# Performance work log

Hardware: AMD Instinct MI355X
Metric: run time of the kernel (lower is better)

## Reference

```python
import jax, jax.numpy as jnp
import numpy as np

GRID_SIZE = 64
THRESHOLD = 1.0
SIGMA = 1.5
K_SHARP = 2.0


def _gaussian_kernel(sigma):
    ksize = max(int(4 * sigma) | 1, 3)
    x = jnp.arange(ksize, dtype=jnp.float32) - ksize // 2
    g1d = jnp.exp(-x ** 2 / (2.0 * sigma ** 2))
    g2d = g1d[None, :] * g1d[:, None]
    g2d = g2d / g2d.sum()
    return g2d[None, None]  # (1,1,k,k) OIHW


def setup_inputs() -> dict:
    key = jax.random.key(0)
    k1, k2, k3, k4 = jax.random.split(key, 4)
    B, V, P, N, MAXP = 4, 512, 8192, 2000, 8
    positions = jax.random.uniform(k1, (B, V, 2), dtype=jnp.float32) * 2.0 - 1.0
    pin_offsets = jax.random.normal(k2, (P, 2), dtype=jnp.float32) * 0.05
    net_to_pin = jax.random.randint(k3, (N, MAXP), 0, P, dtype=jnp.int32)
    pin_to_macro = jax.random.randint(k4, (P,), 0, V, dtype=jnp.int32)
    return {"positions": positions, "pin_offsets": pin_offsets,
            "net_to_pin": net_to_pin, "pin_to_macro": pin_to_macro}


def reference(positions, pin_offsets, net_to_pin, pin_to_macro):
    B = positions.shape[0]
    M = GRID_SIZE
    num_nets = net_to_pin.shape[0]

    # pin positions: (B, P, 2) -- no rotation (rotation_onehot=None branch)
    pin_pos = positions[:, pin_to_macro, :] + pin_offsets[None]

    # per-net bounding boxes over valid pins
    valid = net_to_pin >= 0                                  # (N, maxp)
    safe_idx = jnp.maximum(net_to_pin, 0)
    net_pin_pos = pin_pos[:, safe_idx, :]                    # (B, N, maxp, 2)
    mask = valid[None, :, :, None]
    bbox_max = jnp.max(jnp.where(mask, net_pin_pos, -1e9), axis=2)  # (B, N, 2)
    bbox_min = jnp.min(jnp.where(mask, net_pin_pos, 1e9), axis=2)

    # to grid coordinates
    bbox_max_g = (bbox_max + 1.0) * 0.5 * (M - 1)
    bbox_min_g = (bbox_min + 1.0) * 0.5 * (M - 1)

    # soft rectangular indicators on the MxM grid
    gx = jnp.arange(M, dtype=jnp.float32)
    grid_x, grid_y = jnp.meshgrid(gx, gx, indexing="xy")     # (M, M)
    grid_x = grid_x[None, None]                               # (1,1,M,M)
    grid_y = grid_y[None, None]
    x_min = bbox_min_g[..., 0][..., None, None]               # (B,N,1,1)
    x_max = bbox_max_g[..., 0][..., None, None]
    y_min = bbox_min_g[..., 1][..., None, None]
    y_max = bbox_max_g[..., 1][..., None, None]

    in_x = jax.nn.sigmoid(K_SHARP * (grid_x - x_min + 0.5)) * \
           jax.nn.sigmoid(K_SHARP * (x_max - grid_x + 0.5))
    in_y = jax.nn.sigmoid(K_SHARP * (grid_y - y_min + 0.5)) * \
           jax.nn.sigmoid(K_SHARP * (y_max - grid_y + 0.5))
    indicator = in_x * in_y                                    # (B,N,M,M)

    bbox_size = jnp.maximum((x_max - x_min + 1.0) * (y_max - y_min + 1.0), 1.0)
    rudy = jnp.sum(indicator / bbox_size, axis=1, keepdims=True)  # (B,1,M,M)

    # gaussian smoothing (SAME padding)
    kernel = _gaussian_kernel(SIGMA)
    pad = kernel.shape[-1] // 2
    rudy_smooth = jax.lax.conv_general_dilated(
        rudy, kernel, window_strides=(1, 1),
        padding=((pad, pad), (pad, pad)),
        dimension_numbers=("NCHW", "OIHW", "NCHW"))

    overflow = jax.nn.relu(rudy_smooth - THRESHOLD)
    penalty = jnp.sum(overflow ** 2, axis=(1, 2, 3))           # (B,)
    return penalty, rudy_smooth
```

## Files before the change

kernel.cpp:

```cpp
#include <hip/hip_runtime.h>

#define GRID   64
#define BATCH  4
#define NV     512
#define NP     8192
#define NNET   2000
#define MAXPIN 8
#define NB     125
#define NCHUNK 16
#define CELLS  (GRID * GRID)

__device__ __forceinline__ float sigmoidf_fast(float z) {
    return 1.0f / (1.0f + __expf(-z));
}

__global__ __launch_bounds__(256)
void rudy_partial_kernel(const float* __restrict__ positions,
                         const float* __restrict__ pin_offsets,
                         const int*   __restrict__ net_to_pin,
                         const int*   __restrict__ pin_to_macro,
                         float* __restrict__ partial) {
    const int chunk = blockIdx.x;
    const int b     = blockIdx.y;
    const int t     = threadIdx.x;

    __shared__ float s_inx[NB][GRID];
    __shared__ float s_iny[NB][GRID];
    __shared__ float s_xmin[NB], s_xmax[NB], s_ymin[NB], s_ymax[NB], s_inv[NB];

    if (t < NB) {
        const int n = chunk * NB + t;
        const int4* np4 = (const int4*)(net_to_pin + n * MAXPIN);
        int4 q0 = np4[0], q1 = np4[1];
        int pis[8] = {q0.x, q0.y, q0.z, q0.w, q1.x, q1.y, q1.z, q1.w};
        float xmn = 1e9f, xmx = -1e9f, ymn = 1e9f, ymx = -1e9f;
        const float2* pos2 = (const float2*)positions;
        const float2* off2 = (const float2*)pin_offsets;
        #pragma unroll
        for (int j = 0; j < MAXPIN; ++j) {
            int pi = pis[j];
            int sp = pi > 0 ? pi : 0;
            int v  = pin_to_macro[sp];
            float2 p = pos2[b * NV + v];
            float2 o = off2[sp];
            float px = p.x + o.x, py = p.y + o.y;
            bool valid = pi >= 0;
            float vx_hi = valid ? px : -1e9f, vx_lo = valid ? px : 1e9f;
            float vy_hi = valid ? py : -1e9f, vy_lo = valid ? py : 1e9f;
            xmx = fmaxf(xmx, vx_hi); xmn = fminf(xmn, vx_lo);
            ymx = fmaxf(ymx, vy_hi); ymn = fminf(ymn, vy_lo);
        }
        float xming = (xmn + 1.0f) * 31.5f;
        float xmaxg = (xmx + 1.0f) * 31.5f;
        float yming = (ymn + 1.0f) * 31.5f;
        float ymaxg = (ymx + 1.0f) * 31.5f;
        float size = fmaxf((xmaxg - xming + 1.0f) * (ymaxg - yming + 1.0f), 1.0f);
        s_xmin[t] = xming; s_xmax[t] = xmaxg;
        s_ymin[t] = yming; s_ymax[t] = ymaxg;
        s_inv[t]  = 1.0f / size;
    }
    __syncthreads();

    #pragma unroll
    for (int i = 0; i < 63; ++i) {
        int v = i * 256 + t;
        if (v < NB * 128) {
            int n     = v >> 7;
            int rem   = v & 127;
            int which = rem >> 6;
            int coord = rem & 63;
            float c  = (float)coord;
            float lo = which ? s_ymin[n] : s_xmin[n];
            float hi = which ? s_ymax[n] : s_xmax[n];
            float val = sigmoidf_fast(2.0f * (c - lo + 0.5f)) *
                        sigmoidf_fast(2.0f * (hi - c + 0.5f));
            if (which) s_iny[n][coord] = val; else s_inx[n][coord] = val;
        }
    }
    __syncthreads();

    const int lane = t & 63;
    const int w    = t >> 6;
    float acc[16];
    #pragma unroll
    for (int k = 0; k < 16; ++k) acc[k] = 0.0f;

    #pragma unroll 5
    for (int n = 0; n < NB; ++n) {
        float xv = s_inx[n][lane] * s_inv[n];
        const float4* iny4 = (const float4*)&s_iny[n][w * 16];
        #pragma unroll
        for (int k4 = 0; k4 < 4; ++k4) {
            float4 yv = iny4[k4];
            acc[k4 * 4 + 0] += yv.x * xv;
            acc[k4 * 4 + 1] += yv.y * xv;
            acc[k4 * 4 + 2] += yv.z * xv;
            acc[k4 * 4 + 3] += yv.w * xv;
        }
    }

    float* dst = partial + (b * NCHUNK + chunk) * CELLS;
    #pragma unroll
    for (int k = 0; k < 16; ++k) {
        dst[(w * 16 + k) * GRID + lane] = acc[k];
    }
}

__global__ __launch_bounds__(1024)
void smooth_penalty_kernel(const float* __restrict__ partial,
                           float* __restrict__ out_penalty,
                           float* __restrict__ out_smooth) {
    const int b = blockIdx.x;
    const int t = threadIdx.x;

    __shared__ float tile[CELLS];
    __shared__ float tmp [CELLS];
    __shared__ float red[16];

    float g[7];
    {
        float s = 0.0f;
        #pragma unroll
        for (int i = 0; i < 7; ++i) {
            float d = (float)(i - 3);
            g[i] = expf(-d * d / 4.5f);
            s += g[i];
        }
        float inv = 1.0f / s;
        #pragma unroll
        for (int i = 0; i < 7; ++i) g[i] *= inv;
    }

    const float4* base4 = (const float4*)(partial + b * NCHUNK * CELLS);
    float4 s4 = make_float4(0.0f, 0.0f, 0.0f, 0.0f);
    #pragma unroll
    for (int ch = 0; ch < NCHUNK; ++ch) {
        float4 v = base4[ch * 1024 + t];
        s4.x += v.x; s4.y += v.y; s4.z += v.z; s4.w += v.w;
    }
    ((float4*)tile)[t] = s4;
    __syncthreads();

    #pragma unroll
    for (int k = 0; k < 4; ++k) {
        int c = k * 1024 + t;
        int y = c >> 6, x = c & 63;
        float s = 0.0f;
        #pragma unroll
        for (int d = -3; d <= 3; ++d) {
            int xx = x + d;
            if (xx >= 0 && xx < GRID) s += g[d + 3] * tile[y * GRID + xx];
        }
        tmp[c] = s;
    }
    __syncthreads();

    float local = 0.0f;
    #pragma unroll
    for (int k = 0; k < 4; ++k) {
        int c = k * 1024 + t;
        int y = c >> 6, x = c & 63;
        float s = 0.0f;
        #pragma unroll
        for (int d = -3; d <= 3; ++d) {
            int yy = y + d;
            if (yy >= 0 && yy < GRID) s += g[d + 3] * tmp[yy * GRID + x];
        }
        out_smooth[b * CELLS + c] = s;
        float ov = s - 1.0f;
        ov = ov > 0.0f ? ov : 0.0f;
        local += ov * ov;
    }

    #pragma unroll
    for (int off = 32; off > 0; off >>= 1) local += __shfl_down(local, off, 64);
    if ((t & 63) == 0) red[t >> 6] = local;
    __syncthreads();
    if (t == 0) {
        float s = 0.0f;
        #pragma unroll
        for (int i = 0; i < 16; ++i) s += red[i];
        out_penalty[b] = s;
    }
}

extern "C" void kernel_launch(void* const* d_in, const int* in_sizes, int n_in,
                              void* d_out, int out_size, void* d_ws, size_t ws_size,
                              hipStream_t stream) {
    const float* positions    = (const float*)d_in[0];
    const float* pin_offsets  = (const float*)d_in[1];
    const int*   net_to_pin   = (const int*)d_in[2];
    const int*   pin_to_macro = (const int*)d_in[3];
    float* out     = (float*)d_out;
    float* partial = (float*)d_ws;

    rudy_partial_kernel<<<dim3(NCHUNK, BATCH), 256, 0, stream>>>(
        positions, pin_offsets, net_to_pin, pin_to_macro, partial);
    smooth_penalty_kernel<<<BATCH, 1024, 0, stream>>>(partial, out, out + BATCH);
}
```

Measured before the change: 80.94 us.

## Accumulate per-chunk RUDY maps with global atomics instead of partial buffers

Each net chunk now atomically adds its 64x64 accumulation directly into a single per-batch RUDY map, replacing the 16 separate partial maps. The smoothing kernel no longer reduces those partials and drops from 1024 to 256 threads per block. This cuts partial-buffer writes and reads, but adds a memset launch and contended float atomics (16 blocks per cell), which also make the summation order nondeterministic.

```diff
diff --git a/kernel.cpp b/kernel.cpp
--- a/kernel.cpp
+++ b/kernel.cpp
@@ -15,11 +15,11 @@
 }
 
 __global__ __launch_bounds__(256)
-void rudy_partial_kernel(const float* __restrict__ positions,
-                         const float* __restrict__ pin_offsets,
-                         const int*   __restrict__ net_to_pin,
-                         const int*   __restrict__ pin_to_macro,
-                         float* __restrict__ partial) {
+void rudy_accum_kernel(const float* __restrict__ positions,
+                       const float* __restrict__ pin_offsets,
+                       const int*   __restrict__ net_to_pin,
+                       const int*   __restrict__ pin_to_macro,
+                       float* __restrict__ rudy) {
     const int chunk = blockIdx.x;
     const int b     = blockIdx.y;
     const int t     = threadIdx.x;
@@ -45,10 +45,10 @@
             float2 o = off2[sp];
             float px = p.x + o.x, py = p.y + o.y;
             bool valid = pi >= 0;
-            float vx_hi = valid ? px : -1e9f, vx_lo = valid ? px : 1e9f;
-            float vy_hi = valid ? py : -1e9f, vy_lo = valid ? py : 1e9f;
-            xmx = fmaxf(xmx, vx_hi); xmn = fminf(xmn, vx_lo);
-            ymx = fmaxf(ymx, vy_hi); ymn = fminf(ymn, vy_lo);
+            xmx = fmaxf(xmx, valid ? px : -1e9f);
+            xmn = fminf(xmn, valid ? px :  1e9f);
+            ymx = fmaxf(ymx, valid ? py : -1e9f);
+            ymn = fminf(ymn, valid ? py :  1e9f);
         }
         float xming = (xmn + 1.0f) * 31.5f;
         float xmaxg = (xmx + 1.0f) * 31.5f;
@@ -99,15 +99,15 @@
         }
     }
 
-    float* dst = partial + (b * NCHUNK + chunk) * CELLS;
+    float* dst = rudy + b * CELLS;
     #pragma unroll
     for (int k = 0; k < 16; ++k) {
-        dst[(w * 16 + k) * GRID + lane] = acc[k];
+        atomicAdd(&dst[(w * 16 + k) * GRID + lane], acc[k]);
     }
 }
 
-__global__ __launch_bounds__(1024)
-void smooth_penalty_kernel(const float* __restrict__ partial,
+__global__ __launch_bounds__(256)
+void smooth_penalty_kernel(const float* __restrict__ rudy,
                            float* __restrict__ out_penalty,
                            float* __restrict__ out_smooth) {
     const int b = blockIdx.x;
@@ -115,7 +115,7 @@
 
     __shared__ float tile[CELLS];
     __shared__ float tmp [CELLS];
-    __shared__ float red[16];
+    __shared__ float red[4];
 
     float g[7];
     {
@@ -131,19 +131,15 @@
         for (int i = 0; i < 7; ++i) g[i] *= inv;
     }
 
-    const float4* base4 = (const float4*)(partial + b * NCHUNK * CELLS);
-    float4 s4 = make_float4(0.0f, 0.0f, 0.0f, 0.0f);
+    const float4* src4 = (const float4*)(rudy + b * CELLS);
+    float4* tile4 = (float4*)tile;
     #pragma unroll
-    for (int ch = 0; ch < NCHUNK; ++ch) {
-        float4 v = base4[ch * 1024 + t];
-        s4.x += v.x; s4.y += v.y; s4.z += v.z; s4.w += v.w;
-    }
-    ((float4*)tile)[t] = s4;
+    for (int k = 0; k < 4; ++k) tile4[k * 256 + t] = src4[k * 256 + t];
     __syncthreads();
 
     #pragma unroll
-    for (int k = 0; k < 4; ++k) {
-        int c = k * 1024 + t;
+    for (int k = 0; k < 16; ++k) {
+        int c = k * 256 + t;
         int y = c >> 6, x = c & 63;
         float s = 0.0f;
         #pragma unroll
@@ -157,8 +153,8 @@
 
     float local = 0.0f;
     #pragma unroll
-    for (int k = 0; k < 4; ++k) {
-        int c = k * 1024 + t;
+    for (int k = 0; k < 16; ++k) {
+        int c = k * 256 + t;
         int y = c >> 6, x = c & 63;
         float s = 0.0f;
         #pragma unroll
@@ -176,12 +172,7 @@
     for (int off = 32; off > 0; off >>= 1) local += __shfl_down(local, off, 64);
     if ((t & 63) == 0) red[t >> 6] = local;
     __syncthreads();
-    if (t == 0) {
-        float s = 0.0f;
-        #pragma unroll
-        for (int i = 0; i < 16; ++i) s += red[i];
-        out_penalty[b] = s;
-    }
+    if (t == 0) out_penalty[b] = red[0] + red[1] + red[2] + red[3];
 }
 
 extern "C" void kernel_launch(void* const* d_in, const int* in_sizes, int n_in,
@@ -191,10 +182,11 @@
     const float* pin_offsets  = (const float*)d_in[1];
     const int*   net_to_pin   = (const int*)d_in[2];
     const int*   pin_to_macro = (const int*)d_in[3];
-    float* out     = (float*)d_out;
-    float* partial = (float*)d_ws;
+    float* out  = (float*)d_out;
+    float* rudy = (float*)d_ws;
 
-    rudy_partial_kernel<<<dim3(NCHUNK, BATCH), 256, 0, stream>>>(
-        positions, pin_offsets, net_to_pin, pin_to_macro, partial);
-    smooth_penalty_kernel<<<BATCH, 1024, 0, stream>>>(partial, out, out + BATCH);
+    hipMemsetAsync(d_ws, 0, BATCH * CELLS * sizeof(float), stream);
+    rudy_accum_kernel<<<dim3(NCHUNK, BATCH), 256, 0, stream>>>(
+        positions, pin_offsets, net_to_pin, pin_to_macro, rudy);
+    smooth_penalty_kernel<<<BATCH, 256, 0, stream>>>(rudy, out, out + BATCH);
 }
```

Result: slower. 84.19 us (+4.0%).
